# Kernel optimization log

Measured on AMD Instinct MI355X. Metric: run time of the kernel, lower is better.

The kernel has to match this reference:

```python
import jax, jax.numpy as jnp
import numpy as np

BN_EPS = 1e-5

def setup_inputs() -> dict:
    key = jax.random.key(0)
    ks = jax.random.split(key, 12)
    B, N, C, D = 8, 2048, 768, 384  # batch, tokens, high_dim, low_dim//reduc_ratio
    s_in = 1.0 / np.sqrt(C)
    s_out = 1.0 / np.sqrt(D)
    return {
        "x_h": jax.random.normal(ks[0], (B, N, C), jnp.float32),
        "x_l": jax.random.normal(ks[1], (B, N, C), jnp.float32),
        "w_g": jax.random.normal(ks[2], (D, C), jnp.float32) * s_in,
        "b_g": jax.random.normal(ks[3], (D,), jnp.float32) * s_in,
        "w_theta": jax.random.normal(ks[4], (D, C), jnp.float32) * s_in,
        "b_theta": jax.random.normal(ks[5], (D,), jnp.float32) * s_in,
        "w_phi": jax.random.normal(ks[6], (D, C), jnp.float32) * s_in,
        "b_phi": jax.random.normal(ks[7], (D,), jnp.float32) * s_in,
        "w_out": jax.random.normal(ks[8], (C, D), jnp.float32) * s_out,
        "b_out": jax.random.normal(ks[9], (C,), jnp.float32) * s_out,
        "bn_gamma": jax.random.normal(ks[10], (C,), jnp.float32),
        "bn_beta": jax.random.normal(ks[11], (C,), jnp.float32),
    }

def reference(x_h, x_l, w_g, b_g, w_theta, b_theta, w_phi, b_phi, w_out, b_out, bn_gamma, bn_beta):
    # 1x1 conv1d over channels == per-token linear
    g_x = jnp.einsum('bnc,dc->bnd', x_l, w_g) + b_g          # [B, N_l, D]
    theta_x = jnp.einsum('bnc,dc->bnd', x_h, w_theta) + b_theta  # [B, N_h, D]
    phi_x = jnp.einsum('bnc,dc->bnd', x_l, w_phi) + b_phi    # [B, N_l, D]
    n_l = phi_x.shape[1]
    energy = jnp.einsum('bnd,bmd->bnm', theta_x, phi_x)      # [B, N_h, N_l]
    attention = energy / n_l                                  # scalar normalization
    y = jnp.einsum('bnm,bmd->bnd', attention, g_x)           # [B, N_h, D]
    y = jnp.einsum('bnd,cd->bnc', y, w_out) + b_out          # [B, N_h, C]
    # BatchNorm1d (training mode): per-channel stats over batch and length dims
    mean = jnp.mean(y, axis=(0, 1))
    var = jnp.var(y, axis=(0, 1))
    y = bn_gamma * (y - mean) * jax.lax.rsqrt(var + BN_EPS) + bn_beta
    return y + x_h                                            # [B, N_h, C]
```

## Files before the change

### kernel.cpp

```cpp
#include <hip/hip_runtime.h>

typedef short bf16x8 __attribute__((ext_vector_type(8)));
typedef float f32x4 __attribute__((ext_vector_type(4)));

constexpr int Bb = 8, Ntok = 2048, Cdim = 768, Ddim = 384, Mrows = 16384;
constexpr int KSPLIT = 4;

__device__ __forceinline__ void gload16(const void* g, void* l) {
    __builtin_amdgcn_global_load_lds(
        (const __attribute__((address_space(1))) unsigned int*)g,
        (__attribute__((address_space(3))) unsigned int*)l, 16, 0, 0);
}

__device__ __forceinline__ unsigned short f2bf(float x) {
    union { float f; unsigned u; } c; c.f = x;
    const unsigned r = c.u + 0x7fffu + ((c.u >> 16) & 1u);
    return (unsigned short)(r >> 16);
}
__device__ __forceinline__ float bf2f(unsigned short u) {
    union { unsigned u; float f; } c; c.u = (unsigned)u << 16;
    return c.f;
}
__device__ __forceinline__ uint4 cvt8(const float4 a, const float4 b) {
    union { unsigned short u[8]; uint4 q; } r;
    r.u[0] = f2bf(a.x); r.u[1] = f2bf(a.y); r.u[2] = f2bf(a.z); r.u[3] = f2bf(a.w);
    r.u[4] = f2bf(b.x); r.u[5] = f2bf(b.y); r.u[6] = f2bf(b.z); r.u[7] = f2bf(b.w);
    return r.q;
}

#define ACQ()  do { asm volatile("" ::: "memory"); __builtin_amdgcn_s_barrier(); \
                    asm volatile("" ::: "memory"); } while (0)
#define REL_N() do { asm volatile("" ::: "memory"); __builtin_amdgcn_s_barrier(); \
                     asm volatile("" ::: "memory"); } while (0)

__device__ __forceinline__ void swz_xcd(int& bx, int& by, int& bz) {
    const int NN = gridDim.x, NY = gridDim.y;
    const int NP = NY * gridDim.z;
    const int lin = blockIdx.x + NN * (blockIdx.y + NY * blockIdx.z);
    const int x = lin & 7, g = lin >> 3;
    const int pan = x * (NP >> 3) + g / NN;
    bx = g % NN; by = pan % NY; bz = pan / NY;
}

__global__ __launch_bounds__(256) void cast_xw(
        const float* __restrict__ xl, const float* __restrict__ xh,
        const float* __restrict__ s0, const float* __restrict__ s1,
        const float* __restrict__ s2, const float* __restrict__ s3,
        unsigned short* __restrict__ dxl, unsigned short* __restrict__ dxh,
        unsigned short* __restrict__ d0, unsigned short* __restrict__ d1,
        unsigned short* __restrict__ d2, unsigned short* __restrict__ d3) {
    const int b = blockIdx.x;
    if (b < 576) {
        constexpr int n8 = 294912 / 8;
        const int i = b * 256 + threadIdx.x;
        const int sel = i / n8, loc = i - sel * n8;
        const float* s = sel == 0 ? s0 : sel == 1 ? s1 : sel == 2 ? s2 : s3;
        unsigned short* d = sel == 0 ? d0 : sel == 1 ? d1 : sel == 2 ? d2 : d3;
        const float4* s4 = (const float4*)s;
        ((uint4*)d)[loc] = cvt8(s4[2 * loc], s4[2 * loc + 1]);
    } else if (b < 6720) {
        const int i = (b - 576) * 256 + threadIdx.x;
        const float4* s4 = (const float4*)xl;
        ((uint4*)dxl)[i] = cvt8(s4[2 * i], s4[2 * i + 1]);
    } else {
        const int i = (b - 6720) * 256 + threadIdx.x;
        const float4* s4 = (const float4*)xh;
        ((uint4*)dxh)[i] = cvt8(s4[2 * i], s4[2 * i + 1]);
    }
}

__global__ __launch_bounds__(256) void gemm_inputs(
        const unsigned short* __restrict__ Xh, const unsigned short* __restrict__ Wth,
        const float* __restrict__ bth, unsigned short* __restrict__ Tout,
        const unsigned short* __restrict__ Xl, const unsigned short* __restrict__ Wpg,
        const float* __restrict__ bph, const float* __restrict__ bg,
        unsigned short* __restrict__ PGTout) {
    __shared__ __align__(16) char smem[34304];

    const int tid  = threadIdx.x;
    const int lane = tid & 63;
    const int w    = tid >> 6;
    const int wm   = w >> 1, wn = w & 1;

    const int bid = blockIdx.x;
    const int x   = bid & 7;
    const int g   = bid >> 3;
    const bool isTh = (g < 48);
    int bx, pan;
    if (isTh) { bx = g % 3;                 pan = x * 16 + g / 3; }
    else      { const int l = g - 48; bx = l % 6; pan = x * 16 + l / 6; }
    const int bm = pan * 128, bn = bx * 128;

    const unsigned short* A = isTh ? Xh : Xl;
    const unsigned short* B = isTh ? Wth : Wpg;
    constexpr int K = Cdim;
    constexpr int nt = K / 32;

    const int ldRow = tid >> 2;
    const int ldK   = (tid & 3) * 8;
    const unsigned ldsOff = tid * 16;
    const size_t aOff0 = (size_t)(bm + ldRow) * K + ldK;
    const size_t aOff1 = (size_t)(bm + 64 + ldRow) * K + ldK;
    const size_t bOff0 = (size_t)(bn + ldRow) * K + ldK;
    const size_t bOff1 = (size_t)(bn + 64 + ldRow) * K + ldK;

    f32x4 acc[4][4] = {};
    const int fr = lane & 15;
    const int fh = (lane >> 4) * 16;

    auto bufA = [&](int p) -> char* { return smem + p * 8192; };
    auto bufB = [&](int p) -> char* { return smem + 16384 + p * 8192; };
    auto stage = [&](int p, int k0) {
        gload16(A + aOff0 + k0, bufA(p) + ldsOff);
        gload16(A + aOff1 + k0, bufA(p) + 4096 + ldsOff);
        gload16(B + bOff0 + k0, bufB(p) + ldsOff);
        gload16(B + bOff1 + k0, bufB(p) + 4096 + ldsOff);
    };
    auto compute = [&](int p) {
        const char* smA = bufA(p);
        const char* smB = bufB(p);
        bf16x8 fa[4], fb[4];
#pragma unroll
        for (int m = 0; m < 4; ++m)
            fa[m] = *(const bf16x8*)(smA + (wm * 64 + m * 16 + fr) * 64 + fh);
#pragma unroll
        for (int n = 0; n < 4; ++n)
            fb[n] = *(const bf16x8*)(smB + (wn * 64 + n * 16 + fr) * 64 + fh);
#pragma unroll
        for (int m = 0; m < 4; ++m)
#pragma unroll
            for (int n = 0; n < 4; ++n)
                acc[m][n] = __builtin_amdgcn_mfma_f32_16x16x32_bf16(fa[m], fb[n], acc[m][n], 0, 0, 0);
    };

    stage(0, 0);
    for (int t = 0; t < nt; ++t) {
        const int p = t & 1;
        const bool more = (t + 1) < nt;
        if (more) {
            stage(p ^ 1, (t + 1) * 32);
            asm volatile("s_waitcnt vmcnt(4)" ::: "memory");
        } else {
            asm volatile("s_waitcnt vmcnt(0)" ::: "memory");
        }
        ACQ();
        compute(p);
        REL_N();
    }

    const int r0 = (lane >> 4) * 4;
    const int cc = lane & 15;

    if (isTh) {
        unsigned short* C = Tout;
#pragma unroll
        for (int n = 0; n < 4; ++n) {
            const int col = bn + wn * 64 + n * 16 + cc;
            const float bv = bth[col];
#pragma unroll
            for (int m = 0; m < 4; ++m)
#pragma unroll
                for (int j = 0; j < 4; ++j)
                    C[(size_t)(bm + wm * 64 + m * 16 + r0 + j) * Ddim + col] =
                        f2bf(acc[m][n][j] + bv);
        }
    } else {
        unsigned short* T = (unsigned short*)smem;
#pragma unroll
        for (int n = 0; n < 4; ++n) {
            const int ccol = wn * 64 + n * 16 + cc;
            const int gcol = bn + ccol;
            const float bv = gcol < Ddim ? bph[gcol] : bg[gcol - Ddim];
#pragma unroll
            for (int m = 0; m < 4; ++m)
#pragma unroll
                for (int j = 0; j < 4; ++j)
                    T[ccol * 134 + (wm * 64 + m * 16 + r0 + j)] = f2bf(acc[m][n][j] + bv);
        }
        __syncthreads();
        const int b   = bm >> 11;
        const int bmb = bm & 2047;
        unsigned short* Co = PGTout + (size_t)b * (2 * Ddim) * Ntok;
#pragma unroll
        for (int i = 0; i < 32; ++i) {
            const int d = w * 32 + i;
            const unsigned v = *(const unsigned*)((const char*)smem + d * 268 + lane * 4);
            *(unsigned*)(Co + (size_t)(bn + d) * Ntok + bmb + lane * 2) = v;
        }
    }
}

template <int OMODE, int SPLITK>
__global__ __launch_bounds__(256) void gemm_bf16(
        const unsigned short* __restrict__ Abase, long sA,
        const unsigned short* __restrict__ Bbase, long sB,
        const float* __restrict__ bias, const float* __restrict__ bias2, int Nsplit,
        void* __restrict__ Cbase, long sC,
        int M, int N, int K, float scale,
        float* __restrict__ psumG, float* __restrict__ psqG) {
    __shared__ __align__(16) char smem[32768];

    int bxi, byi, bzi;
    swz_xcd(bxi, byi, bzi);

    const int tid  = threadIdx.x;
    const int lane = tid & 63;
    const int w    = tid >> 6;
    const int wm   = w >> 1, wn = w & 1;
    const int bm = byi * 128, bn = bxi * 128;
    const int zz = bzi;

    int zb, kStart, kEnd;
    if constexpr (SPLITK > 0) {
        zb = zz / SPLITK;
        const int kl = K / SPLITK;
        kStart = (zz % SPLITK) * kl;
        kEnd = kStart + kl;
    } else {
        zb = zz; kStart = 0; kEnd = K;
    }

    const unsigned short* A = Abase + (size_t)zb * sA;
    const unsigned short* B = Bbase + (size_t)zb * sB;

    const int ldRow = tid >> 2;
    const int ldK   = (tid & 3) * 8;
    const unsigned ldsOff = tid * 16;
    const size_t aOff0 = (size_t)(bm + ldRow) * K + ldK;
    const size_t aOff1 = (size_t)(bm + 64 + ldRow) * K + ldK;
    const size_t bOff0 = (size_t)(bn + ldRow) * K + ldK;
    const size_t bOff1 = (size_t)(bn + 64 + ldRow) * K + ldK;

    f32x4 acc[4][4] = {};
    const int fr = lane & 15;
    const int fh = (lane >> 4) * 16;

    auto bufA = [&](int p) -> char* { return smem + p * 8192; };
    auto bufB = [&](int p) -> char* { return smem + 16384 + p * 8192; };
    auto stage = [&](int p, int k0) {
        gload16(A + aOff0 + k0, bufA(p) + ldsOff);
        gload16(A + aOff1 + k0, bufA(p) + 4096 + ldsOff);
        gload16(B + bOff0 + k0, bufB(p) + ldsOff);
        gload16(B + bOff1 + k0, bufB(p) + 4096 + ldsOff);
    };
    auto compute = [&](int p) {
        const char* smA = bufA(p);
        const char* smB = bufB(p);
        bf16x8 fa[4], fb[4];
#pragma unroll
        for (int m = 0; m < 4; ++m)
            fa[m] = *(const bf16x8*)(smA + (wm * 64 + m * 16 + fr) * 64 + fh);
#pragma unroll
        for (int n = 0; n < 4; ++n)
            fb[n] = *(const bf16x8*)(smB + (wn * 64 + n * 16 + fr) * 64 + fh);
#pragma unroll
        for (int m = 0; m < 4; ++m)
#pragma unroll
            for (int n = 0; n < 4; ++n)
                acc[m][n] = __builtin_amdgcn_mfma_f32_16x16x32_bf16(fa[m], fb[n], acc[m][n], 0, 0, 0);
    };

    const int nt = (kEnd - kStart) >> 5;
    stage(0, kStart);
    for (int t = 0; t < nt; ++t) {
        const int p = t & 1;
        const bool more = (t + 1) < nt;
        if (more) {
            stage(p ^ 1, kStart + (t + 1) * 32);
            asm volatile("s_waitcnt vmcnt(4)" ::: "memory");
        } else {
            asm volatile("s_waitcnt vmcnt(0)" ::: "memory");
        }
        ACQ();
        compute(p);
        REL_N();
    }

    const int r0 = (lane >> 4) * 4;
    const int cc = lane & 15;
    auto getbias = [&](int gcol) -> float {
        if (!bias) return 0.0f;
        return gcol < Nsplit ? bias[gcol] : bias2[gcol - Nsplit];
    };

    if constexpr (OMODE == 0) {
        float* C = (float*)Cbase + (size_t)(SPLITK > 0 ? zz : zb) * sC;
#pragma unroll
        for (int n = 0; n < 4; ++n) {
            const int col = bn + wn * 64 + n * 16 + cc;
            const float bv = getbias(col);
#pragma unroll
            for (int m = 0; m < 4; ++m)
#pragma unroll
                for (int j = 0; j < 4; ++j)
                    C[(size_t)(bm + wm * 64 + m * 16 + r0 + j) * N + col] = acc[m][n][j] + bv;
        }
    } else if constexpr (OMODE == 1) {
        unsigned short* C = (unsigned short*)Cbase + (size_t)(SPLITK > 0 ? zz : zb) * sC;
#pragma unroll
        for (int n = 0; n < 4; ++n) {
            const int col = bn + wn * 64 + n * 16 + cc;
            const float bv = getbias(col);
#pragma unroll
            for (int m = 0; m < 4; ++m)
#pragma unroll
                for (int j = 0; j < 4; ++j)
                    C[(size_t)(bm + wm * 64 + m * 16 + r0 + j) * N + col] =
                        f2bf(acc[m][n][j] * scale + bv);
        }
    } else {
        unsigned short* C = (unsigned short*)Cbase + (size_t)zb * sC;
        float colS[4], colQ[4];
#pragma unroll
        for (int n = 0; n < 4; ++n) {
            const int col = bn + wn * 64 + n * 16 + cc;
            const float bv = getbias(col);
            float s = 0.f, q = 0.f;
#pragma unroll
            for (int m = 0; m < 4; ++m)
#pragma unroll
                for (int j = 0; j < 4; ++j) {
                    const float v = acc[m][n][j] + bv;
                    C[(size_t)(bm + wm * 64 + m * 16 + r0 + j) * N + col] = f2bf(v);
                    s += v; q = fmaf(v, v, q);
                }
            s += __shfl_xor(s, 16); s += __shfl_xor(s, 32);
            q += __shfl_xor(q, 16); q += __shfl_xor(q, 32);
            colS[n] = s; colQ[n] = q;
        }
        float* sums = (float*)smem;
        float* sqs  = sums + 256;
        if (lane < 16) {
#pragma unroll
            for (int n = 0; n < 4; ++n) {
                sums[wm * 128 + wn * 64 + n * 16 + cc] = colS[n];
                sqs [wm * 128 + wn * 64 + n * 16 + cc] = colQ[n];
            }
        }
        __syncthreads();
        if (tid < 128) {
            const int slot = zb * gridDim.y + byi;
            psumG[(size_t)slot * Cdim + bn + tid] = sums[tid] + sums[128 + tid];
            psqG [(size_t)slot * Cdim + bn + tid] = sqs[tid]  + sqs[128 + tid];
        }
    }
}

__global__ __launch_bounds__(256) void reduce_mt(const float* __restrict__ part,
                                                 unsigned short* __restrict__ Mo) {
    const int i = blockIdx.x * 256 + threadIdx.x;
    const int e = i * 4;
    const int b = e / (Ddim * Ddim);
    const int r = e - b * (Ddim * Ddim);
    const float* base = part + (size_t)b * KSPLIT * (Ddim * Ddim) + r;
    float4 s = *(const float4*)(base);
    const float4 s1 = *(const float4*)(base + 1 * Ddim * Ddim);
    const float4 s2 = *(const float4*)(base + 2 * Ddim * Ddim);
    const float4 s3 = *(const float4*)(base + 3 * Ddim * Ddim);
    s.x += s1.x + s2.x + s3.x; s.y += s1.y + s2.y + s3.y;
    s.z += s1.z + s2.z + s3.z; s.w += s1.w + s2.w + s3.w;
    constexpr float sc = 1.0f / (float)Ntok;
    union { unsigned short u[4]; uint2 q; } o;
    o.u[0] = f2bf(s.x * sc); o.u[1] = f2bf(s.y * sc);
    o.u[2] = f2bf(s.z * sc); o.u[3] = f2bf(s.w * sc);
    *(uint2*)(Mo + e) = o.q;
}

__global__ __launch_bounds__(256) void bn_finalize(const float* __restrict__ psum,
                                                   const float* __restrict__ psq,
                                                   const float* __restrict__ gamma,
                                                   const float* __restrict__ beta,
                                                   float* __restrict__ a,
                                                   float* __restrict__ bb) {
    const int c = blockIdx.x * 256 + threadIdx.x;
    if (c >= Cdim) return;
    float s = 0.f, q = 0.f;
    for (int b = 0; b < 128; ++b) { s += psum[(size_t)b * Cdim + c]; q += psq[(size_t)b * Cdim + c]; }
    const float mean = s * (1.0f / (float)Mrows);
    const float var  = fmaf(-mean, mean, q * (1.0f / (float)Mrows));
    const float inv  = rsqrtf(var + 1e-5f);
    const float gsc  = gamma[c] * inv;
    a[c]  = gsc;
    bb[c] = fmaf(-mean, gsc, beta[c]);
}

__global__ __launch_bounds__(256) void bn_apply(const unsigned short* __restrict__ y,
                                                const float* __restrict__ xh,
                                                const float* __restrict__ a,
                                                const float* __restrict__ bb,
                                                float* __restrict__ outp) {
    const size_t i = (size_t)blockIdx.x * 256 + threadIdx.x;
    union { uint4 q; unsigned short u[8]; } v; v.q = ((const uint4*)y)[i];
    const int c8 = (int)(i % (Cdim / 8));
    const float4 A0 = ((const float4*)a)[c8 * 2],  A1 = ((const float4*)a)[c8 * 2 + 1];
    const float4 B0 = ((const float4*)bb)[c8 * 2], B1 = ((const float4*)bb)[c8 * 2 + 1];
    const float4 X0 = ((const float4*)xh)[i * 2],  X1 = ((const float4*)xh)[i * 2 + 1];
    float4 o0, o1;
    o0.x = fmaf(A0.x, bf2f(v.u[0]), B0.x) + X0.x;
    o0.y = fmaf(A0.y, bf2f(v.u[1]), B0.y) + X0.y;
    o0.z = fmaf(A0.z, bf2f(v.u[2]), B0.z) + X0.z;
    o0.w = fmaf(A0.w, bf2f(v.u[3]), B0.w) + X0.w;
    o1.x = fmaf(A1.x, bf2f(v.u[4]), B1.x) + X1.x;
    o1.y = fmaf(A1.y, bf2f(v.u[5]), B1.y) + X1.y;
    o1.z = fmaf(A1.z, bf2f(v.u[6]), B1.z) + X1.z;
    o1.w = fmaf(A1.w, bf2f(v.u[7]), B1.w) + X1.w;
    ((float4*)outp)[i * 2]     = o0;
    ((float4*)outp)[i * 2 + 1] = o1;
}

extern "C" void kernel_launch(void* const* d_in, const int* in_sizes, int n_in,
                              void* d_out, int out_size, void* d_ws, size_t ws_size,
                              hipStream_t stream) {
    const float* x_h   = (const float*)d_in[0];
    const float* x_l   = (const float*)d_in[1];
    const float* w_g   = (const float*)d_in[2];
    const float* b_g   = (const float*)d_in[3];
    const float* w_th  = (const float*)d_in[4];
    const float* b_th  = (const float*)d_in[5];
    const float* w_ph  = (const float*)d_in[6];
    const float* b_ph  = (const float*)d_in[7];
    const float* w_out = (const float*)d_in[8];
    const float* b_out = (const float*)d_in[9];
    const float* gamma = (const float*)d_in[10];
    const float* beta  = (const float*)d_in[11];
    float* out = (float*)d_out;

    char* p = (char*)d_ws;
    unsigned short* Scr   = (unsigned short*)p; p += (size_t)Mrows * Cdim * 2;
    unsigned short* Wth16 = (unsigned short*)p; p += 294912 * 2;
    unsigned short* Wpg16 = (unsigned short*)p; p += 2 * 294912 * 2;
    unsigned short* Wout16= (unsigned short*)p; p += 294912 * 2;
    unsigned short* Tbuf  = (unsigned short*)p; p += (size_t)Mrows * Ddim * 2;
    unsigned short* PGT   = (unsigned short*)p; p += (size_t)Mrows * Cdim * 2;
    unsigned short* Mbuf  = (unsigned short*)p; p += (size_t)Bb * Ddim * Ddim * 2;
    unsigned short* QTbuf = (unsigned short*)p; p += (size_t)Bb * Cdim * Ddim * 2;
    float* psum = (float*)p; p += (size_t)128 * Cdim * 4;
    float* psq  = (float*)p; p += (size_t)128 * Cdim * 4;
    float* avec = (float*)p; p += Cdim * 4;
    float* bvec = (float*)p; p += Cdim * 4;
    unsigned short* Xl16 = Scr;
    float* part = (float*)Scr;
    unsigned short* Ybuf = Scr;
    unsigned short* Xh16 = (unsigned short*)d_out;

    dim3 blk(256);
    const int BIG = 1 << 30;

    cast_xw<<<12864, blk, 0, stream>>>(x_l, x_h, w_th, w_ph, w_g, w_out,
                                       Xl16, Xh16, Wth16, Wpg16, Wpg16 + 294912, Wout16);
    gemm_inputs<<<1152, blk, 0, stream>>>(
        Xh16, Wth16, b_th, Tbuf,
        Xl16, Wpg16, b_ph, b_g, PGT);
    gemm_bf16<0, KSPLIT><<<dim3(3, 3, Bb * KSPLIT), blk, 0, stream>>>(
        PGT, (long)2 * Ddim * Ntok,
        PGT + (size_t)Ddim * Ntok, (long)2 * Ddim * Ntok, nullptr, nullptr, BIG,
        part, (long)Ddim * Ddim, Ddim, Ddim, Ntok, 1.0f, nullptr, nullptr);
    reduce_mt<<<1152, blk, 0, stream>>>(part, Mbuf);
    gemm_bf16<1, 0><<<dim3(3, 6, 8), blk, 0, stream>>>(
        Wout16, 0, Mbuf, (long)Ddim * Ddim, nullptr, nullptr, BIG,
        QTbuf, (long)Cdim * Ddim, Cdim, Ddim, Ddim, 1.0f, nullptr, nullptr);
    gemm_bf16<3, 0><<<dim3(6, 16, 8), blk, 0, stream>>>(
        Tbuf, (long)Ntok * Ddim, QTbuf, (long)Cdim * Ddim, b_out, nullptr, BIG,
        Ybuf, (long)Ntok * Cdim, Ntok, Cdim, Ddim, 1.0f, psum, psq);
    bn_finalize<<<dim3(3), blk, 0, stream>>>(psum, psq, gamma, beta, avec, bvec);
    bn_apply<<<dim3(6144), blk, 0, stream>>>(Ybuf, x_h, avec, bvec, out);
}
```

Before: 148.6 us.

## Switch GEMM main loops to triple-buffered LDS with one barrier per step

New measurement: 149.1 us. No clear change (+0.3%).

```diff
diff --git a/kernel.cpp b/kernel.cpp
--- a/kernel.cpp
+++ b/kernel.cpp
@@ -28,10 +28,8 @@
     return r.q;
 }
 
-#define ACQ()  do { asm volatile("" ::: "memory"); __builtin_amdgcn_s_barrier(); \
-                    asm volatile("" ::: "memory"); } while (0)
-#define REL_N() do { asm volatile("" ::: "memory"); __builtin_amdgcn_s_barrier(); \
-                     asm volatile("" ::: "memory"); } while (0)
+#define BAR() do { asm volatile("" ::: "memory"); __builtin_amdgcn_s_barrier(); \
+                   asm volatile("" ::: "memory"); } while (0)
 
 __device__ __forceinline__ void swz_xcd(int& bx, int& by, int& bz) {
     const int NN = gridDim.x, NY = gridDim.y;
@@ -75,7 +73,7 @@
         const unsigned short* __restrict__ Xl, const unsigned short* __restrict__ Wpg,
         const float* __restrict__ bph, const float* __restrict__ bg,
         unsigned short* __restrict__ PGTout) {
-    __shared__ __align__(16) char smem[34304];
+    __shared__ __align__(16) char smem[49152];
 
     const int tid  = threadIdx.x;
     const int lane = tid & 63;
@@ -109,8 +107,9 @@
     const int fh = (lane >> 4) * 16;
 
     auto bufA = [&](int p) -> char* { return smem + p * 8192; };
-    auto bufB = [&](int p) -> char* { return smem + 16384 + p * 8192; };
-    auto stage = [&](int p, int k0) {
+    auto bufB = [&](int p) -> char* { return smem + 24576 + p * 8192; };
+    auto stage = [&](int p, int t) {
+        const int k0 = t * 32;
         gload16(A + aOff0 + k0, bufA(p) + ldsOff);
         gload16(A + aOff1 + k0, bufA(p) + 4096 + ldsOff);
         gload16(B + bOff0 + k0, bufB(p) + ldsOff);
@@ -133,19 +132,15 @@
                 acc[m][n] = __builtin_amdgcn_mfma_f32_16x16x32_bf16(fa[m], fb[n], acc[m][n], 0, 0, 0);
     };
 
-    stage(0, 0);
+    stage(0, 0); stage(1, 1);
+    int p = 0;
     for (int t = 0; t < nt; ++t) {
-        const int p = t & 1;
-        const bool more = (t + 1) < nt;
-        if (more) {
-            stage(p ^ 1, (t + 1) * 32);
-            asm volatile("s_waitcnt vmcnt(4)" ::: "memory");
-        } else {
-            asm volatile("s_waitcnt vmcnt(0)" ::: "memory");
-        }
-        ACQ();
+        if (t + 1 < nt) asm volatile("s_waitcnt vmcnt(4)" ::: "memory");
+        else            asm volatile("s_waitcnt vmcnt(0)" ::: "memory");
+        BAR();
+        if (t + 2 < nt) stage(p == 0 ? 2 : p - 1, t + 2);
         compute(p);
-        REL_N();
+        p = (p == 2) ? 0 : p + 1;
     }
 
     const int r0 = (lane >> 4) * 4;
@@ -165,6 +160,7 @@
                         f2bf(acc[m][n][j] + bv);
         }
     } else {
+        __syncthreads();
         unsigned short* T = (unsigned short*)smem;
 #pragma unroll
         for (int n = 0; n < 4; ++n) {
@@ -198,7 +194,7 @@
         void* __restrict__ Cbase, long sC,
         int M, int N, int K, float scale,
         float* __restrict__ psumG, float* __restrict__ psqG) {
-    __shared__ __align__(16) char smem[32768];
+    __shared__ __align__(16) char smem[49152];
 
     int bxi, byi, bzi;
     swz_xcd(bxi, byi, bzi);
@@ -236,8 +232,9 @@
     const int fh = (lane >> 4) * 16;
 
     auto bufA = [&](int p) -> char* { return smem + p * 8192; };
-    auto bufB = [&](int p) -> char* { return smem + 16384 + p * 8192; };
-    auto stage = [&](int p, int k0) {
+    auto bufB = [&](int p) -> char* { return smem + 24576 + p * 8192; };
+    auto stage = [&](int p, int t) {
+        const int k0 = kStart + t * 32;
         gload16(A + aOff0 + k0, bufA(p) + ldsOff);
         gload16(A + aOff1 + k0, bufA(p) + 4096 + ldsOff);
         gload16(B + bOff0 + k0, bufB(p) + ldsOff);
@@ -261,19 +258,15 @@
     };
 
     const int nt = (kEnd - kStart) >> 5;
-    stage(0, kStart);
+    stage(0, 0); stage(1, 1);
+    int p = 0;
     for (int t = 0; t < nt; ++t) {
-        const int p = t & 1;
-        const bool more = (t + 1) < nt;
-        if (more) {
-            stage(p ^ 1, kStart + (t + 1) * 32);
-            asm volatile("s_waitcnt vmcnt(4)" ::: "memory");
-        } else {
-            asm volatile("s_waitcnt vmcnt(0)" ::: "memory");
-        }
-        ACQ();
+        if (t + 1 < nt) asm volatile("s_waitcnt vmcnt(4)" ::: "memory");
+        else            asm volatile("s_waitcnt vmcnt(0)" ::: "memory");
+        BAR();
+        if (t + 2 < nt) stage(p == 0 ? 2 : p - 1, t + 2);
         compute(p);
-        REL_N();
+        p = (p == 2) ? 0 : p + 1;
     }
 
     const int r0 = (lane >> 4) * 4;
@@ -328,6 +321,7 @@
             q += __shfl_xor(q, 16); q += __shfl_xor(q, 32);
             colS[n] = s; colQ[n] = q;
         }
+        __syncthreads();
         float* sums = (float*)smem;
         float* sqs  = sums + 256;
         if (lane < 16) {
```
